# Performance work log

Hardware: AMD Instinct MI355X
Metric: run time of the kernel (lower is better)

Reference implementation:

```python
import jax, jax.numpy as jnp
import numpy as np

NB_HEADS = 16
HEAD_DIM = 64
ATTN_LIM = 1024   # L: span of attention over past tokens
BLOCK = 512       # M: query block size
RAMP = 32         # attn_span_len: soft-mask ramp length
BATCH = 8         # sequences; merged leading dim is BATCH*NB_HEADS


def _skew(X, pad_value):
    # X: B x M x L  ->  B x M x (M+L), row i shifted right by i
    B, M, L = X.shape
    X = jnp.pad(X, ((0, 0), (0, 0), (0, M + 1)), constant_values=pad_value)
    X = X.reshape(B, M * (L + M + 1))[:, :-M]
    return X.reshape(B, M, M + L)


def _unskew(X):
    # X: B x M x (M+L)  ->  B x M x L, undo the diagonal shift
    B, M, ML = X.shape
    L = ML - M
    X = X.reshape(B, M * ML)
    X = jnp.pad(X, ((0, 0), (0, M)))
    X = X.reshape(B, M, ML + 1)
    return X[:, :, :L]


def setup_inputs() -> dict:
    key = jax.random.key(0)
    ks = jax.random.split(key, 5)
    B = BATCH * NB_HEADS
    M, L, H = BLOCK, ATTN_LIM, HEAD_DIM
    return {
        "query": jax.random.normal(ks[0], (B, M, H), jnp.float32),
        "key": jax.random.normal(ks[1], (B, M + L, H), jnp.float32),
        "value": jax.random.normal(ks[2], (B, M + L, H), jnp.float32),
        "key_pe": jax.random.normal(ks[3], (1, H, L), jnp.float32),
        "span_val": jax.random.uniform(ks[4], (NB_HEADS, 1, 1), jnp.float32),
    }


def reference(query, key, value, key_pe, span_val):
    B, M, H = query.shape
    L = key_pe.shape[-1]
    # content attention over the (M+L) cache window, unskewed to relative coords
    attn_cont = _unskew(jnp.matmul(query, jnp.swapaxes(key, -1, -2)))  # B x M x L
    attn_pos = jnp.matmul(query, key_pe)                               # B x M x L
    attn = (attn_cont + attn_pos) / jnp.sqrt(jnp.float32(H))
    attn = jax.nn.softmax(attn, axis=-1)
    # adaptive-span soft mask per head (AdaptiveMask), then renormalize
    z = jnp.clip(span_val, 0.0, 1.0)
    template = jnp.arange(1 - L, 1, dtype=jnp.float32)    # linspace(1-L, 0, L)
    mask = jnp.clip((template + z * jnp.float32(L)) / jnp.float32(RAMP) + 1.0,
                    0.0, 1.0)
    attn = attn.reshape(B // NB_HEADS, NB_HEADS, M, L) * mask[None]
    attn = attn / (attn.sum(-1, keepdims=True) + 1e-8)
    attn = attn.reshape(B, M, L)
    # skew back to absolute coords and contract with values
    out = jnp.matmul(_skew(attn, 0.0), value)             # B x M x H
    return out
```

## Files before the change

### kernel.cpp

```cpp
#include <hip/hip_runtime.h>
#include <hip/hip_bf16.h>

typedef __attribute__((ext_vector_type(8))) short short8;
typedef __attribute__((ext_vector_type(4))) float f32x4;

#define MFMA16(a, b, c) __builtin_amdgcn_mfma_f32_16x16x32_bf16((a), (b), (c), 0, 0, 0)
#define QSCALE 0.18033688f
#define EXP2F(x) __builtin_amdgcn_exp2f(x)

__device__ __forceinline__ unsigned short f2bf(float f) {
    unsigned u = __builtin_bit_cast(unsigned, f);
    u += 0x7FFFu + ((u >> 16) & 1u);
    return (unsigned short)(u >> 16);
}
__device__ __forceinline__ unsigned short bfc(float f) {
    return (unsigned short)((__builtin_bit_cast(unsigned, f) + 0x8000u) >> 16);
}

__device__ __forceinline__ short8 pack8(float4 a, float4 b) {
    short8 r;
    r[0] = (short)f2bf(a.x); r[1] = (short)f2bf(a.y);
    r[2] = (short)f2bf(a.z); r[3] = (short)f2bf(a.w);
    r[4] = (short)f2bf(b.x); r[5] = (short)f2bf(b.y);
    r[6] = (short)f2bf(b.z); r[7] = (short)f2bf(b.w);
    return r;
}
__device__ __forceinline__ short8 pack8s(float4 a, float4 b, float s) {
    short8 r;
    r[0] = (short)f2bf(a.x * s); r[1] = (short)f2bf(a.y * s);
    r[2] = (short)f2bf(a.z * s); r[3] = (short)f2bf(a.w * s);
    r[4] = (short)f2bf(b.x * s); r[5] = (short)f2bf(b.y * s);
    r[6] = (short)f2bf(b.z * s); r[7] = (short)f2bf(b.w * s);
    return r;
}

__device__ __forceinline__ void stage16(const void* g, void* l) {
    __builtin_amdgcn_global_load_lds((const __attribute__((address_space(1))) void*)g,
                                     (__attribute__((address_space(3))) void*)l, 16, 0, 0);
}
__device__ __forceinline__ float bpermf(int sa, float v) {
    return __builtin_bit_cast(float,
        __builtin_amdgcn_ds_bpermute(sa, __builtin_bit_cast(int, v)));
}

__global__ void conv_all_kernel(const float* __restrict__ K, const float* __restrict__ V,
                                const float* __restrict__ PE,
                                unsigned short* __restrict__ Kws,
                                unsigned short* __restrict__ Vws,
                                unsigned short* __restrict__ PET) {
    __shared__ unsigned short T[64][72];
    const int blk = blockIdx.x, tid = threadIdx.x;
    if (blk < 6144) {
        int idx = blk * 256 + tid;
        int jl = idx >> 3;
        int e0 = (idx & 7) << 3;
        int x  = (jl & 7) << 3;
        const float* src = K + ((size_t)jl << 6) + (e0 ^ x);
        float4 a = ((const float4*)src)[0], b = ((const float4*)src)[1];
        *(short8*)(Kws + ((size_t)jl << 6) + e0) = pack8(a, b);
    } else if (blk < 9216) {
        int blkv = blk - 6144;
        int b = blkv / 24, vb = blkv - b * 24;
        {
            int j = tid >> 2, h0 = (tid & 3) << 4;
            const float* src = V + ((size_t)(b * 1536 + vb * 64 + j) << 6) + h0;
            float4 a0 = ((const float4*)src)[0], a1 = ((const float4*)src)[1];
            float4 a2 = ((const float4*)src)[2], a3 = ((const float4*)src)[3];
            *(short8*)&T[j][h0]     = pack8(a0, a1);
            *(short8*)&T[j][h0 + 8] = pack8(a2, a3);
        }
        __syncthreads();
        {
            int h = tid & 63, k0 = (tid >> 6) << 4;
            int x = (h & 7) << 3;
            unsigned short* dst = Vws + ((size_t)(b * 24 + vb) << 12) + (h << 6) + k0;
            short8 o0, o1;
#pragma unroll
            for (int u = 0; u < 8; ++u) o0[u] = (short)T[(k0 + u) ^ x][h];
#pragma unroll
            for (int u = 0; u < 8; ++u) o1[u] = (short)T[(k0 + 8 + u) ^ x][h];
            ((short8*)dst)[0] = o0;
            ((short8*)dst)[1] = o1;
        }
    } else {
        int idx = (blk - 9216) * 256 + tid;
        int l = idx >> 6, h = idx & 63;
        PET[idx] = f2bf(PE[(h << 10) | l]);
    }
}

__global__ void pe_only_kernel(const float* __restrict__ pe,
                               unsigned short* __restrict__ pet) {
    int idx = blockIdx.x * 256 + threadIdx.x;
    int l = idx >> 6, h = idx & 63;
    pet[idx] = f2bf(pe[(h << 10) | l]);
}

__global__ __launch_bounds__(256, 4) void attn_v10(
    const float* __restrict__ Qg, const unsigned short* __restrict__ Kws,
    const unsigned short* __restrict__ Vws, const unsigned short* __restrict__ PET,
    const float* __restrict__ SPAN, float* __restrict__ OUT)
{
    __shared__ unsigned short Klds[2][4096];
    __shared__ unsigned short Vlds[2][4096];

    const int bid = blockIdx.x;
    const int b   = (bid & 7) * 16 + (bid >> 6);
    const int i0  = ((bid >> 3) & 7) << 6;
    const int tid = threadIdx.x, w = tid >> 6, lane = tid & 63;
    const int c16 = lane & 15, g = lane >> 4;

    float z = SPAN[b & 15];
    z = fminf(fmaxf(z, 0.f), 1.f);
    const float mc = z * 32.f + 1.f - 1023.f * 0.03125f;

    int t_start = (int)floorf(14.46f - 16.f * z) + 1;
    if (t_start < 0) t_start = 0;

    short8 qf0, qf1;
    {
        const float* qp = Qg + ((size_t)((b << 9) + i0 + (w << 4) + c16) << 6) + (g << 3);
        qf0 = pack8s(*(const float4*)qp,        *(const float4*)(qp + 4),  QSCALE);
        qf1 = pack8s(*(const float4*)(qp + 32), *(const float4*)(qp + 36), QSCALE);
    }

    const f32x4 zero = {0.f, 0.f, 0.f, 0.f};
    f32x4 Oacc[4] = {zero, zero, zero, zero};
    f32x4 sumw = zero, sume = zero;
    f32x4 Sp[5];

    const char* kbase = (const char*)Kws + (((size_t)b * 1536 + i0) << 7);
    const char* vbase = (const char*)Vws + (((size_t)b * 24 + (i0 >> 6)) << 13);
    const int ubase = w << 10;
    const int loff  = ubase + lane * 16;

    int bsrc[4];
#pragma unroll
    for (int r = 0; r < 4; ++r)
        bsrc[r] = ((lane & 48) | ((c16 - (g << 2) - r) & 15)) << 2;

#define STAGE(bufi, t) do {                                                    \
        const char* kg_ = kbase + (t) * 8192 + loff;                           \
        const char* vg_ = vbase + (t) * 8192 + loff;                           \
        unsigned short* kl_ = &Klds[bufi][ubase >> 1];                         \
        unsigned short* vl_ = &Vlds[bufi][ubase >> 1];                         \
        stage16(kg_, kl_); stage16(kg_ + 4096, kl_ + 2048);                    \
        stage16(vg_, vl_); stage16(vg_ + 4096, vl_ + 2048);                    \
    } while (0)

#define STRIP(dst, lbase) do {                                                 \
        int lr_ = (lbase) + c16;                                               \
        lr_ = lr_ < 0 ? 0 : (lr_ > 1023 ? 1023 : lr_);                         \
        const unsigned short* pp_ = PET + ((lr_ << 6) + (g << 3));             \
        short8 p0_ = *(const short8*)pp_;                                      \
        short8 p1_ = *(const short8*)(pp_ + 32);                               \
        f32x4 a_ = MFMA16(qf0, p0_, zero);                                     \
        dst = MFMA16(qf1, p1_, a_);                                            \
    } while (0)

    STAGE(t_start & 1, t_start);
    { const int lb0 = (t_start << 6) - (w << 4) - 16; STRIP(Sp[4], lb0); }

    for (int t = t_start; t < 17; ++t) {
        const int buf = t & 1;
        __syncthreads();
        if (t < 16) STAGE(buf ^ 1, t + 1);

        const int d0w = (t << 6) - (w << 4);
        const int lb  = d0w - 16;
        const bool edge = (t == 0) || (t == 16);

        __builtin_amdgcn_s_setprio(1);
        f32x4 Sc[4];
        const int xk = (c16 & 7) << 3;
#pragma unroll
        for (int jc = 0; jc < 4; ++jc) {
            const unsigned short* p = &Klds[buf][(jc * 16 + c16) << 6];
            short8 k0 = *(const short8*)(p + ((g << 3) ^ xk));
            short8 k1 = *(const short8*)(p + (((g << 3) + 32) ^ xk));
            f32x4 a = MFMA16(qf0, k0, zero);
            Sc[jc] = MFMA16(qf1, k1, a);
        }
        Sp[0] = Sp[4];
        STRIP(Sp[1], lb + 16);
        STRIP(Sp[2], lb + 32);
        STRIP(Sp[3], lb + 48);
        STRIP(Sp[4], lb + 64);
        __builtin_amdgcn_s_setprio(0);

        asm volatile("s_waitcnt lgkmcnt(0)" ::: "memory");
        __builtin_amdgcn_sched_barrier(0);
        __builtin_amdgcn_s_barrier();
        __builtin_amdgcn_sched_barrier(0);

        unsigned short* Wp = &Klds[buf][w << 10];
#pragma unroll
        for (int r = 0; r < 4; ++r) {
            const int ii    = (g << 2) + r;
            const int delta = c16 - ii;
            const int sa    = bsrc[r];
            float sh0 = bpermf(sa, Sp[0][r]);
            float sh1 = bpermf(sa, Sp[1][r]);
            float sh2 = bpermf(sa, Sp[2][r]);
            float sh3 = bpermf(sa, Sp[3][r]);
            float sh4 = bpermf(sa, Sp[4][r]);
            const bool lo_ = delta < 0;
            const int xw = (ii & 7) << 3;
            const int lbase = d0w + delta;
            const float mb = fmaf((float)lbase, 0.03125f, mc);
#pragma unroll
            for (int jc = 0; jc < 4; ++jc) {
                float pa, pb;
                if (jc == 0) { pa = sh0; pb = sh1; }
                else if (jc == 1) { pa = sh1; pb = sh2; }
                else if (jc == 2) { pa = sh2; pb = sh3; }
                else { pa = sh3; pb = sh4; }
                const float pe = lo_ ? pa : pb;
                float e = EXP2F(Sc[jc][r] + pe);
                if (edge) {
                    const int l_ = lbase + (jc << 4);
                    if ((unsigned)l_ >= 1024u) e = 0.f;
                }
                const float m_ = fminf(fmaxf(mb + 0.5f * jc, 0.f), 1.f);
                const float wgt = e * m_;
                sumw[r] += wgt;
                sume[r] += e;
                Wp[(ii << 6) + (((jc << 4) + c16) ^ xw)] = bfc(wgt);
            }
        }

        const int xr = (c16 & 7) << 3;
        const unsigned short* wrow = Wp + (c16 << 6);
        short8 wf0 = *(const short8*)(wrow + ((g << 3) ^ xr));
        short8 wf1 = *(const short8*)(wrow + (((g << 3) + 32) ^ xr));
        __builtin_amdgcn_s_setprio(1);
#pragma unroll
        for (int ht = 0; ht < 4; ++ht) {
            const unsigned short* vr = &Vlds[buf][(ht * 16 + c16) << 6];
            short8 v0 = *(const short8*)(vr + ((g << 3) ^ xr));
            short8 v1 = *(const short8*)(vr + (((g << 3) + 32) ^ xr));
            f32x4 a = MFMA16(wf0, v0, Oacc[ht]);
            Oacc[ht] = MFMA16(wf1, v1, a);
        }
        __builtin_amdgcn_s_setprio(0);
    }

#pragma unroll
    for (int r = 0; r < 4; ++r) {
        float sw = sumw[r], se = sume[r];
#pragma unroll
        for (int m = 1; m < 16; m <<= 1) {
            sw += __shfl_xor(sw, m, 64);
            se += __shfl_xor(se, m, 64);
        }
        const float inv = 1.0f / (sw + 1e-8f * se);
        float* op = OUT + ((size_t)((b << 9) + i0 + (w << 4) + (g << 2) + r) << 6);
#pragma unroll
        for (int ht = 0; ht < 4; ++ht)
            op[ht * 16 + c16] = Oacc[ht][r] * inv;
    }
#undef STAGE
#undef STRIP
}

__global__ __launch_bounds__(256, 4) void attn_v1(
    const float* __restrict__ Qg, const float* __restrict__ Kg,
    const float* __restrict__ Vg, const unsigned short* __restrict__ PET,
    const float* __restrict__ SPAN, float* __restrict__ OUT)
{
    __shared__ unsigned short Klds[64 * 72];
    __shared__ unsigned short Vlds[64 * 72];
    __shared__ unsigned short Wlds[4][16 * 72];

    const int bid = blockIdx.x;
    const int b  = (bid & 7) * 16 + (bid >> 6);
    const int qt = (bid >> 3) & 7;
    const int i0 = qt << 6;
    const int tid = threadIdx.x, w = tid >> 6, lane = tid & 63;
    const int c16 = lane & 15, g = lane >> 4;

    float z = SPAN[b & 15];
    z = fminf(fmaxf(z, 0.0f), 1.0f);
    const float zc = z * 32.0f + 1.0f;

    short8 qf0, qf1;
    {
        const float* qp = Qg + ((size_t)(b * 512 + i0 + w * 16 + c16) * 64 + g * 8);
        qf0 = pack8(*(const float4*)qp,        *(const float4*)(qp + 4));
        qf1 = pack8(*(const float4*)(qp + 32), *(const float4*)(qp + 36));
    }
    const f32x4 zero = {0.f, 0.f, 0.f, 0.f};
    f32x4 Oacc[4] = {zero, zero, zero, zero};
    f32x4 sumw = zero, sume = zero;
    const int d0w_off = -(w << 4);

    for (int dblk = 0; dblk < 17; ++dblk) {
        const int d = dblk << 6;
        __syncthreads();
        {
            const int row = tid >> 2, h0 = (tid & 3) << 4;
            const float* kp = Kg + ((size_t)(b * 1536 + i0 + d + row) * 64 + h0);
            float4 k0 = ((const float4*)kp)[0], k1 = ((const float4*)kp)[1];
            float4 k2 = ((const float4*)kp)[2], k3 = ((const float4*)kp)[3];
            *(short8*)&Klds[row * 72 + h0]     = pack8(k0, k1);
            *(short8*)&Klds[row * 72 + h0 + 8] = pack8(k2, k3);
        }
        {
            const int j0 = (tid & 31) << 1, h0 = (tid >> 5) << 3;
            const float* vp = Vg + ((size_t)(b * 1536 + i0 + d + j0) * 64 + h0);
            float4 a0 = ((const float4*)vp)[0], a1 = ((const float4*)vp)[1];
            float4 b0 = ((const float4*)(vp + 64))[0], b1 = ((const float4*)(vp + 64))[1];
            float ta[8] = {a0.x, a0.y, a0.z, a0.w, a1.x, a1.y, a1.z, a1.w};
            float tb[8] = {b0.x, b0.y, b0.z, b0.w, b1.x, b1.y, b1.z, b1.w};
#pragma unroll
            for (int u = 0; u < 8; ++u) {
                unsigned pv = (unsigned)f2bf(ta[u]) | ((unsigned)f2bf(tb[u]) << 16);
                *(unsigned*)&Vlds[(h0 + u) * 72 + j0] = pv;
            }
        }
        __syncthreads();

        const int d0w = d + d0w_off;
        const int lb  = d0w - 16;
        f32x4 Sp[5];
#pragma unroll
        for (int tt = 0; tt < 5; ++tt) {
            int lr = lb + (tt << 4) + c16;
            lr = lr < 0 ? 0 : (lr > 1023 ? 1023 : lr);
            const unsigned short* pp = PET + ((lr << 6) + (g << 3));
            short8 p0 = *(const short8*)pp;
            short8 p1 = *(const short8*)(pp + 32);
            f32x4 acc = MFMA16(qf0, p0, zero);
            Sp[tt] = MFMA16(qf1, p1, acc);
        }
        f32x4 Sc[4];
#pragma unroll
        for (int jc = 0; jc < 4; ++jc) {
            const unsigned short* kb = &Klds[(jc * 16 + c16) * 72 + (g << 3)];
            short8 k0 = *(const short8*)kb;
            short8 k1 = *(const short8*)(kb + 32);
            f32x4 acc = MFMA16(qf0, k0, zero);
            Sc[jc] = MFMA16(qf1, k1, acc);
        }
        unsigned short* Wp = Wlds[w];
#pragma unroll
        for (int jc = 0; jc < 4; ++jc) {
#pragma unroll
            for (int r = 0; r < 4; ++r) {
                const int ii    = (g << 2) + r;
                const int delta = c16 - ii;
                const int src   = (lane & 48) | (delta & 15);
                const float pa  = __shfl(Sp[jc][r],     src, 64);
                const float pb  = __shfl(Sp[jc + 1][r], src, 64);
                const float pe  = (delta >= 0) ? pb : pa;
                const int l     = d0w + (jc << 4) + delta;
                const float sv  = (Sc[jc][r] + pe) * 0.125f;
                const float e   = __expf(sv);
                const bool valid = ((unsigned)l < 1024u);
                float msk = (float)(l - 1023) * 0.03125f + zc;
                msk = fminf(fmaxf(msk, 0.0f), 1.0f);
                const float wgt = valid ? e * msk : 0.0f;
                sumw[r] += wgt;
                sume[r] += valid ? e : 0.0f;
                Wp[ii * 72 + (jc << 4) + c16] = f2bf(wgt);
            }
        }
        short8 wf0 = *(const short8*)&Wp[c16 * 72 + (g << 3)];
        short8 wf1 = *(const short8*)&Wp[c16 * 72 + 32 + (g << 3)];
#pragma unroll
        for (int ht = 0; ht < 4; ++ht) {
            const unsigned short* vb = &Vlds[(ht * 16 + c16) * 72 + (g << 3)];
            short8 v0 = *(const short8*)vb;
            short8 v1 = *(const short8*)(vb + 32);
            f32x4 a = MFMA16(wf0, v0, Oacc[ht]);
            Oacc[ht] = MFMA16(wf1, v1, a);
        }
    }
#pragma unroll
    for (int r = 0; r < 4; ++r) {
        float sw = sumw[r], se = sume[r];
#pragma unroll
        for (int m = 1; m < 16; m <<= 1) {
            sw += __shfl_xor(sw, m, 64);
            se += __shfl_xor(se, m, 64);
        }
        const float inv = 1.0f / (sw + 1e-8f * se);
        float* op = OUT + ((size_t)(b * 512 + i0 + w * 16 + (g << 2) + r) * 64);
#pragma unroll
        for (int ht = 0; ht < 4; ++ht)
            op[ht * 16 + c16] = Oacc[ht][r] * inv;
    }
}

extern "C" void kernel_launch(void* const* d_in, const int* in_sizes, int n_in,
                              void* d_out, int out_size, void* d_ws, size_t ws_size,
                              hipStream_t stream) {
    const float* Q    = (const float*)d_in[0];
    const float* K    = (const float*)d_in[1];
    const float* V    = (const float*)d_in[2];
    const float* PE   = (const float*)d_in[3];
    const float* SPAN = (const float*)d_in[4];

    const size_t VWS  = (size_t)128 * 24 * 4096 * 2;
    const size_t KWS  = (size_t)128 * 1536 * 64 * 2;
    const size_t PETB = (size_t)1024 * 64 * 2;
    const size_t NEED = VWS + KWS + PETB;

    if (ws_size >= NEED) {
        unsigned short* Vws = (unsigned short*)d_ws;
        unsigned short* Kws = (unsigned short*)((char*)d_ws + VWS);
        unsigned short* PET = (unsigned short*)((char*)d_ws + VWS + KWS);
        conv_all_kernel<<<9472, 256, 0, stream>>>(K, V, PE, Kws, Vws, PET);
        attn_v10<<<1024, 256, 0, stream>>>(Q, Kws, Vws, PET, SPAN, (float*)d_out);
    } else {
        unsigned short* PET = (unsigned short*)d_ws;
        pe_only_kernel<<<256, 256, 0, stream>>>(PE, PET);
        attn_v1<<<1024, 256, 0, stream>>>(Q, K, V, PET, SPAN, (float*)d_out);
    }
}
```

Before: 95.34 us.

## Split attention into single-wave blocks with 32-key tiles and transposed V layout

The attention kernel moves from 256-thread blocks, where four waves shared 64-key K/V tiles, to 64-thread single-wave blocks that each handle 16 query rows and step over 32-key tiles. Because each block is one wave, the block barriers become plain waitcnts. V is now stored as an h-major transposed workspace that is swizzled when staged. The aim is to remove barrier stalls, give finer-grained scheduling, and start the span-limited loop more tightly, at the cost of each wave loading its own K/V tiles (less reuse and more global/L2 traffic) and issuing more loop iterations.

```diff
diff --git a/kernel.cpp b/kernel.cpp
--- a/kernel.cpp
+++ b/kernel.cpp
@@ -46,7 +46,7 @@
 __global__ void conv_all_kernel(const float* __restrict__ K, const float* __restrict__ V,
                                 const float* __restrict__ PE,
                                 unsigned short* __restrict__ Kws,
-                                unsigned short* __restrict__ Vws,
+                                unsigned short* __restrict__ Vws2,
                                 unsigned short* __restrict__ PET) {
     __shared__ unsigned short T[64][72];
     const int blk = blockIdx.x, tid = threadIdx.x;
@@ -71,14 +71,13 @@
         }
         __syncthreads();
         {
-            int h = tid & 63, k0 = (tid >> 6) << 4;
-            int x = (h & 7) << 3;
-            unsigned short* dst = Vws + ((size_t)(b * 24 + vb) << 12) + (h << 6) + k0;
+            int h = tid >> 2, k0 = (tid & 3) << 4;
+            unsigned short* dst = Vws2 + ((size_t)(b * 64 + h)) * 1536 + vb * 64 + k0;
             short8 o0, o1;
 #pragma unroll
-            for (int u = 0; u < 8; ++u) o0[u] = (short)T[(k0 + u) ^ x][h];
-#pragma unroll
-            for (int u = 0; u < 8; ++u) o1[u] = (short)T[(k0 + 8 + u) ^ x][h];
+            for (int u = 0; u < 8; ++u) o0[u] = (short)T[k0 + u][h];
+#pragma unroll
+            for (int u = 0; u < 8; ++u) o1[u] = (short)T[k0 + 8 + u][h];
             ((short8*)dst)[0] = o0;
             ((short8*)dst)[1] = o1;
         }
@@ -96,30 +95,29 @@
     pet[idx] = f2bf(pe[(h << 10) | l]);
 }
 
-__global__ __launch_bounds__(256, 4) void attn_v10(
+__global__ __launch_bounds__(64, 4) void attn_v11(
     const float* __restrict__ Qg, const unsigned short* __restrict__ Kws,
-    const unsigned short* __restrict__ Vws, const unsigned short* __restrict__ PET,
+    const unsigned short* __restrict__ Vws2, const unsigned short* __restrict__ PET,
     const float* __restrict__ SPAN, float* __restrict__ OUT)
 {
-    __shared__ unsigned short Klds[2][4096];
-    __shared__ unsigned short Vlds[2][4096];
+    __shared__ unsigned short Klds[2][2048];
+    __shared__ unsigned short Vlds[2][2048];
 
     const int bid = blockIdx.x;
-    const int b   = (bid & 7) * 16 + (bid >> 6);
-    const int i0  = ((bid >> 3) & 7) << 6;
-    const int tid = threadIdx.x, w = tid >> 6, lane = tid & 63;
+    const int x = bid & 7, y = (bid >> 3) & 15, u = bid >> 7;
+    const int b = x * 16 + y;
+    const int lane = threadIdx.x;
     const int c16 = lane & 15, g = lane >> 4;
 
     float z = SPAN[b & 15];
     z = fminf(fmaxf(z, 0.f), 1.f);
     const float mc = z * 32.f + 1.f - 1023.f * 0.03125f;
-
-    int t_start = (int)floorf(14.46f - 16.f * z) + 1;
-    if (t_start < 0) t_start = 0;
+    int t0 = (int)floorf(29.99f - 32.f * z) + 1;
+    if (t0 < 0) t0 = 0;
 
     short8 qf0, qf1;
     {
-        const float* qp = Qg + ((size_t)((b << 9) + i0 + (w << 4) + c16) << 6) + (g << 3);
+        const float* qp = Qg + ((size_t)((b << 9) + (u << 4) + c16) << 6) + (g << 3);
         qf0 = pack8s(*(const float4*)qp,        *(const float4*)(qp + 4),  QSCALE);
         qf1 = pack8s(*(const float4*)(qp + 32), *(const float4*)(qp + 36), QSCALE);
     }
@@ -127,25 +125,32 @@
     const f32x4 zero = {0.f, 0.f, 0.f, 0.f};
     f32x4 Oacc[4] = {zero, zero, zero, zero};
     f32x4 sumw = zero, sume = zero;
-    f32x4 Sp[5];
-
-    const char* kbase = (const char*)Kws + (((size_t)b * 1536 + i0) << 7);
-    const char* vbase = (const char*)Vws + (((size_t)b * 24 + (i0 >> 6)) << 13);
-    const int ubase = w << 10;
-    const int loff  = ubase + lane * 16;
-
+    f32x4 Sp[3];
+
+    const char* kbase = (const char*)Kws + (((size_t)b * 1536 + (u << 4)) << 7);
+    const unsigned short* vb0 = Vws2 + (size_t)b * 98304;
+    int voff[4];
+#pragma unroll
+    for (int c = 0; c < 4; ++c) {
+        int o  = c * 1024 + lane * 16;
+        int h  = o >> 6;
+        int kk = (o & 63) >> 1;
+        voff[c] = h * 1536 + (kk ^ ((h & 3) << 3));
+    }
     int bsrc[4];
 #pragma unroll
     for (int r = 0; r < 4; ++r)
         bsrc[r] = ((lane & 48) | ((c16 - (g << 2) - r) & 15)) << 2;
 
 #define STAGE(bufi, t) do {                                                    \
-        const char* kg_ = kbase + (t) * 8192 + loff;                           \
-        const char* vg_ = vbase + (t) * 8192 + loff;                           \
-        unsigned short* kl_ = &Klds[bufi][ubase >> 1];                         \
-        unsigned short* vl_ = &Vlds[bufi][ubase >> 1];                         \
-        stage16(kg_, kl_); stage16(kg_ + 4096, kl_ + 2048);                    \
-        stage16(vg_, vl_); stage16(vg_ + 4096, vl_ + 2048);                    \
+        const char* kg_ = kbase + (t) * 4096 + lane * 16;                      \
+        const int  js_ = (u << 4) + ((t) << 5);                                \
+        _Pragma("unroll")                                                      \
+        for (int c_ = 0; c_ < 4; ++c_) {                                       \
+            stage16(kg_ + c_ * 1024, (char*)Klds[bufi] + c_ * 1024);           \
+            stage16((const char*)(vb0 + voff[c_] + js_),                       \
+                    (char*)Vlds[bufi] + c_ * 1024);                            \
+        }                                                                      \
     } while (0)
 
 #define STRIP(dst, lbase) do {                                                 \
@@ -158,42 +163,37 @@
         dst = MFMA16(qf1, p1_, a_);                                            \
     } while (0)
 
-    STAGE(t_start & 1, t_start);
-    { const int lb0 = (t_start << 6) - (w << 4) - 16; STRIP(Sp[4], lb0); }
-
-    for (int t = t_start; t < 17; ++t) {
+    STAGE(t0 & 1, t0);
+    STRIP(Sp[2], (t0 << 5) - 16);
+
+    for (int t = t0; t <= 32; ++t) {
         const int buf = t & 1;
-        __syncthreads();
-        if (t < 16) STAGE(buf ^ 1, t + 1);
-
-        const int d0w = (t << 6) - (w << 4);
-        const int lb  = d0w - 16;
-        const bool edge = (t == 0) || (t == 16);
+        asm volatile("s_waitcnt vmcnt(0)" ::: "memory");
+        __builtin_amdgcn_sched_barrier(0);
+        asm volatile("s_waitcnt lgkmcnt(0)" ::: "memory");
+        __builtin_amdgcn_sched_barrier(0);
+        if (t < 32) STAGE(buf ^ 1, t + 1);
+
+        const int d0 = t << 5;
+        const bool edge = (t == 0) || (t == 32);
 
         __builtin_amdgcn_s_setprio(1);
-        f32x4 Sc[4];
+        f32x4 Sc[2];
         const int xk = (c16 & 7) << 3;
 #pragma unroll
-        for (int jc = 0; jc < 4; ++jc) {
+        for (int jc = 0; jc < 2; ++jc) {
             const unsigned short* p = &Klds[buf][(jc * 16 + c16) << 6];
             short8 k0 = *(const short8*)(p + ((g << 3) ^ xk));
             short8 k1 = *(const short8*)(p + (((g << 3) + 32) ^ xk));
             f32x4 a = MFMA16(qf0, k0, zero);
             Sc[jc] = MFMA16(qf1, k1, a);
         }
-        Sp[0] = Sp[4];
-        STRIP(Sp[1], lb + 16);
-        STRIP(Sp[2], lb + 32);
-        STRIP(Sp[3], lb + 48);
-        STRIP(Sp[4], lb + 64);
+        Sp[0] = Sp[2];
+        STRIP(Sp[1], d0);
+        STRIP(Sp[2], d0 + 16);
         __builtin_amdgcn_s_setprio(0);
 
-        asm volatile("s_waitcnt lgkmcnt(0)" ::: "memory");
-        __builtin_amdgcn_sched_barrier(0);
-        __builtin_amdgcn_s_barrier();
-        __builtin_amdgcn_sched_barrier(0);
-
-        unsigned short* Wp = &Klds[buf][w << 10];
+        unsigned short* Wp = &Klds[buf][0];
 #pragma unroll
         for (int r = 0; r < 4; ++r) {
             const int ii    = (g << 2) + r;
@@ -202,19 +202,14 @@
             float sh0 = bpermf(sa, Sp[0][r]);
             float sh1 = bpermf(sa, Sp[1][r]);
             float sh2 = bpermf(sa, Sp[2][r]);
-            float sh3 = bpermf(sa, Sp[3][r]);
-            float sh4 = bpermf(sa, Sp[4][r]);
             const bool lo_ = delta < 0;
-            const int xw = (ii & 7) << 3;
-            const int lbase = d0w + delta;
+            const int xw = (ii & 3) << 3;
+            const int lbase = d0 + delta;
             const float mb = fmaf((float)lbase, 0.03125f, mc);
 #pragma unroll
-            for (int jc = 0; jc < 4; ++jc) {
-                float pa, pb;
-                if (jc == 0) { pa = sh0; pb = sh1; }
-                else if (jc == 1) { pa = sh1; pb = sh2; }
-                else if (jc == 2) { pa = sh2; pb = sh3; }
-                else { pa = sh3; pb = sh4; }
+            for (int jc = 0; jc < 2; ++jc) {
+                const float pa = (jc == 0) ? sh0 : sh1;
+                const float pb = (jc == 0) ? sh1 : sh2;
                 const float pe = lo_ ? pa : pb;
                 float e = EXP2F(Sc[jc][r] + pe);
                 if (edge) {
@@ -225,22 +220,19 @@
                 const float wgt = e * m_;
                 sumw[r] += wgt;
                 sume[r] += e;
-                Wp[(ii << 6) + (((jc << 4) + c16) ^ xw)] = bfc(wgt);
+                Wp[(ii << 5) + (((jc << 4) + c16) ^ xw)] = bfc(wgt);
             }
         }
 
-        const int xr = (c16 & 7) << 3;
-        const unsigned short* wrow = Wp + (c16 << 6);
-        short8 wf0 = *(const short8*)(wrow + ((g << 3) ^ xr));
-        short8 wf1 = *(const short8*)(wrow + (((g << 3) + 32) ^ xr));
+        const int xr = (c16 & 3) << 3;
+        short8 wf = *(const short8*)(Wp + (c16 << 5) + ((g << 3) ^ xr));
         __builtin_amdgcn_s_setprio(1);
 #pragma unroll
         for (int ht = 0; ht < 4; ++ht) {
-            const unsigned short* vr = &Vlds[buf][(ht * 16 + c16) << 6];
-            short8 v0 = *(const short8*)(vr + ((g << 3) ^ xr));
-            short8 v1 = *(const short8*)(vr + (((g << 3) + 32) ^ xr));
-            f32x4 a = MFMA16(wf0, v0, Oacc[ht]);
-            Oacc[ht] = MFMA16(wf1, v1, a);
+            const int h = ht * 16 + c16;
+            const unsigned short* vr = &Vlds[buf][(h << 5) + ((g << 3) ^ ((h & 3) << 3))];
+            short8 v0 = *(const short8*)vr;
+            Oacc[ht] = MFMA16(wf, v0, Oacc[ht]);
         }
         __builtin_amdgcn_s_setprio(0);
     }
@@ -254,7 +246,7 @@
             se += __shfl_xor(se, m, 64);
         }
         const float inv = 1.0f / (sw + 1e-8f * se);
-        float* op = OUT + ((size_t)((b << 9) + i0 + (w << 4) + (g << 2) + r) << 6);
+        float* op = OUT + ((size_t)((b << 9) + (u << 4) + (g << 2) + r) << 6);
 #pragma unroll
         for (int ht = 0; ht < 4; ++ht)
             op[ht * 16 + c16] = Oacc[ht][r] * inv;
@@ -313,9 +305,9 @@
             float ta[8] = {a0.x, a0.y, a0.z, a0.w, a1.x, a1.y, a1.z, a1.w};
             float tb[8] = {b0.x, b0.y, b0.z, b0.w, b1.x, b1.y, b1.z, b1.w};
 #pragma unroll
-            for (int u = 0; u < 8; ++u) {
-                unsigned pv = (unsigned)f2bf(ta[u]) | ((unsigned)f2bf(tb[u]) << 16);
-                *(unsigned*)&Vlds[(h0 + u) * 72 + j0] = pv;
+            for (int uu = 0; uu < 8; ++uu) {
+                unsigned pv = (unsigned)f2bf(ta[uu]) | ((unsigned)f2bf(tb[uu]) << 16);
+                *(unsigned*)&Vlds[(h0 + uu) * 72 + j0] = pv;
             }
         }
         __syncthreads();
@@ -401,17 +393,17 @@
     const float* PE   = (const float*)d_in[3];
     const float* SPAN = (const float*)d_in[4];
 
-    const size_t VWS  = (size_t)128 * 24 * 4096 * 2;
+    const size_t VWS  = (size_t)128 * 64 * 1536 * 2;
     const size_t KWS  = (size_t)128 * 1536 * 64 * 2;
     const size_t PETB = (size_t)1024 * 64 * 2;
     const size_t NEED = VWS + KWS + PETB;
 
     if (ws_size >= NEED) {
-        unsigned short* Vws = (unsigned short*)d_ws;
-        unsigned short* Kws = (unsigned short*)((char*)d_ws + VWS);
-        unsigned short* PET = (unsigned short*)((char*)d_ws + VWS + KWS);
-        conv_all_kernel<<<9472, 256, 0, stream>>>(K, V, PE, Kws, Vws, PET);
-        attn_v10<<<1024, 256, 0, stream>>>(Q, Kws, Vws, PET, SPAN, (float*)d_out);
+        unsigned short* Vws2 = (unsigned short*)d_ws;
+        unsigned short* Kws  = (unsigned short*)((char*)d_ws + VWS);
+        unsigned short* PET  = (unsigned short*)((char*)d_ws + VWS + KWS);
+        conv_all_kernel<<<9472, 256, 0, stream>>>(K, V, PE, Kws, Vws2, PET);
+        attn_v11<<<4096, 64, 0, stream>>>(Q, Kws, Vws2, PET, SPAN, (float*)d_out);
     } else {
         unsigned short* PET = (unsigned short*)d_ws;
         pe_only_kernel<<<256, 256, 0, stream>>>(PE, PET);
```

New measurement: 123.2 us. +29.2%, slower.

## Skip converting masked-out K/V tiles and use separate LDS for weights

Applied to the files above, without the earlier changes.

The conversion kernel now reads the per-head span and returns early for K and V tiles that lie entirely before the attention kernel's first live tile, so it avoids converting cache regions whose mask weight is zero. The attention kernel writes softmax weights into a dedicated per-wave LDS buffer instead of reusing the K buffer. That removes the mid-iteration block barrier and the wait on LDS counters, and the setprio hints are dropped too. The cost is extra LDS per block, which may reduce occupancy. Tiles that are skipped stay unwritten in the workspace, which is only safe because the attention kernel never reads them.

```diff
diff --git a/kernel.cpp b/kernel.cpp
--- a/kernel.cpp
+++ b/kernel.cpp
@@ -7,6 +7,11 @@
 #define MFMA16(a, b, c) __builtin_amdgcn_mfma_f32_16x16x32_bf16((a), (b), (c), 0, 0, 0)
 #define QSCALE 0.18033688f
 #define EXP2F(x) __builtin_amdgcn_exp2f(x)
+
+__device__ __forceinline__ int tstart_of(float z) {
+    int t = (int)floorf(14.46f - 16.f * z) + 1;
+    return t < 0 ? 0 : t;
+}
 
 __device__ __forceinline__ unsigned short f2bf(float f) {
     unsigned u = __builtin_bit_cast(unsigned, f);
@@ -45,22 +50,31 @@
 
 __global__ void conv_all_kernel(const float* __restrict__ K, const float* __restrict__ V,
                                 const float* __restrict__ PE,
+                                const float* __restrict__ SPAN,
                                 unsigned short* __restrict__ Kws,
                                 unsigned short* __restrict__ Vws,
                                 unsigned short* __restrict__ PET) {
     __shared__ unsigned short T[64][72];
     const int blk = blockIdx.x, tid = threadIdx.x;
     if (blk < 6144) {
+        int b   = blk / 48;
+        int j_hi = (blk - b * 48) * 32 + 31;
+        float z = SPAN[b & 15];
+        z = fminf(fmaxf(z, 0.f), 1.f);
+        if (j_hi < (tstart_of(z) << 6)) return;
         int idx = blk * 256 + tid;
         int jl = idx >> 3;
         int e0 = (idx & 7) << 3;
         int x  = (jl & 7) << 3;
         const float* src = K + ((size_t)jl << 6) + (e0 ^ x);
-        float4 a = ((const float4*)src)[0], b = ((const float4*)src)[1];
-        *(short8*)(Kws + ((size_t)jl << 6) + e0) = pack8(a, b);
+        float4 a = ((const float4*)src)[0], bb = ((const float4*)src)[1];
+        *(short8*)(Kws + ((size_t)jl << 6) + e0) = pack8(a, bb);
     } else if (blk < 9216) {
         int blkv = blk - 6144;
         int b = blkv / 24, vb = blkv - b * 24;
+        float z = SPAN[b & 15];
+        z = fminf(fmaxf(z, 0.f), 1.f);
+        if (vb * 64 + 63 < (tstart_of(z) << 6)) return;
         {
             int j = tid >> 2, h0 = (tid & 3) << 4;
             const float* src = V + ((size_t)(b * 1536 + vb * 64 + j) << 6) + h0;
@@ -96,13 +110,14 @@
     pet[idx] = f2bf(pe[(h << 10) | l]);
 }
 
-__global__ __launch_bounds__(256, 4) void attn_v10(
+__global__ __launch_bounds__(256, 4) void attn_v13(
     const float* __restrict__ Qg, const unsigned short* __restrict__ Kws,
     const unsigned short* __restrict__ Vws, const unsigned short* __restrict__ PET,
     const float* __restrict__ SPAN, float* __restrict__ OUT)
 {
     __shared__ unsigned short Klds[2][4096];
     __shared__ unsigned short Vlds[2][4096];
+    __shared__ unsigned short Wlds[4][1024];
 
     const int bid = blockIdx.x;
     const int b   = (bid & 7) * 16 + (bid >> 6);
@@ -113,9 +128,7 @@
     float z = SPAN[b & 15];
     z = fminf(fmaxf(z, 0.f), 1.f);
     const float mc = z * 32.f + 1.f - 1023.f * 0.03125f;
-
-    int t_start = (int)floorf(14.46f - 16.f * z) + 1;
-    if (t_start < 0) t_start = 0;
+    const int t_start = tstart_of(z);
 
     short8 qf0, qf1;
     {
@@ -170,7 +183,6 @@
         const int lb  = d0w - 16;
         const bool edge = (t == 0) || (t == 16);
 
-        __builtin_amdgcn_s_setprio(1);
         f32x4 Sc[4];
         const int xk = (c16 & 7) << 3;
 #pragma unroll
@@ -186,14 +198,8 @@
         STRIP(Sp[2], lb + 32);
         STRIP(Sp[3], lb + 48);
         STRIP(Sp[4], lb + 64);
-        __builtin_amdgcn_s_setprio(0);
-
-        asm volatile("s_waitcnt lgkmcnt(0)" ::: "memory");
-        __builtin_amdgcn_sched_barrier(0);
-        __builtin_amdgcn_s_barrier();
-        __builtin_amdgcn_sched_barrier(0);
-
-        unsigned short* Wp = &Klds[buf][w << 10];
+
+        unsigned short* Wp = &Wlds[w][0];
 #pragma unroll
         for (int r = 0; r < 4; ++r) {
             const int ii    = (g << 2) + r;
@@ -233,7 +239,6 @@
         const unsigned short* wrow = Wp + (c16 << 6);
         short8 wf0 = *(const short8*)(wrow + ((g << 3) ^ xr));
         short8 wf1 = *(const short8*)(wrow + (((g << 3) + 32) ^ xr));
-        __builtin_amdgcn_s_setprio(1);
 #pragma unroll
         for (int ht = 0; ht < 4; ++ht) {
             const unsigned short* vr = &Vlds[buf][(ht * 16 + c16) << 6];
@@ -242,7 +247,6 @@
             f32x4 a = MFMA16(wf0, v0, Oacc[ht]);
             Oacc[ht] = MFMA16(wf1, v1, a);
         }
-        __builtin_amdgcn_s_setprio(0);
     }
 
 #pragma unroll
@@ -410,8 +414,8 @@
         unsigned short* Vws = (unsigned short*)d_ws;
         unsigned short* Kws = (unsigned short*)((char*)d_ws + VWS);
         unsigned short* PET = (unsigned short*)((char*)d_ws + VWS + KWS);
-        conv_all_kernel<<<9472, 256, 0, stream>>>(K, V, PE, Kws, Vws, PET);
-        attn_v10<<<1024, 256, 0, stream>>>(Q, Kws, Vws, PET, SPAN, (float*)d_out);
+        conv_all_kernel<<<9472, 256, 0, stream>>>(K, V, PE, SPAN, Kws, Vws, PET);
+        attn_v13<<<1024, 256, 0, stream>>>(Q, Kws, Vws, PET, SPAN, (float*)d_out);
     } else {
         unsigned short* PET = (unsigned short*)d_ws;
         pe_only_kernel<<<256, 256, 0, stream>>>(PE, PET);
```

Result: faster. 87.86 us (median of 3 runs) (-7.9%).
